# Performance work log

Hardware: AMD Instinct MI355X
Metric: run time of the kernel (lower is better)

## Reference

```python
import jax, jax.numpy as jnp
import numpy as np

N, E, D, D_NODE, D_EDGE, T, L = 100000, 640000, 128, 128, 32, 8, 3
EPS = 1e-5


def _layernorm(x, g, b):
    m = jnp.mean(x, -1, keepdims=True)
    v = jnp.mean((x - m) ** 2, -1, keepdims=True)
    return (x - m) * jax.lax.rsqrt(v + EPS) * g + b


def setup_inputs() -> dict:
    key = jax.random.key(0)
    ks = jax.random.split(key, 24)
    s = 0.02
    inp = {
        "x": jax.random.normal(ks[0], (N, D_NODE), jnp.float32),
        "edge_index": jax.random.randint(ks[1], (2, E), 0, N, jnp.int64),
        "edge_attr": jax.random.normal(ks[2], (E, D_EDGE), jnp.float32),
        "node_w": jax.random.normal(ks[3], (D_NODE, D), jnp.float32) * s,
        "node_b": jnp.zeros((D,), jnp.float32),
        "edge_w": jax.random.normal(ks[4], (D_EDGE, D), jnp.float32) * s,
        "edge_b": jnp.zeros((D,), jnp.float32),
        "msg_w1": jax.random.normal(ks[5], (L, D, D), jnp.float32) * s,
        "msg_b1": jnp.zeros((L, D), jnp.float32),
        "msg_w2": jax.random.normal(ks[6], (L, D, D), jnp.float32) * s,
        "msg_b2": jnp.zeros((L, D), jnp.float32),
        "upd_w1": jax.random.normal(ks[7], (L, D, 2 * D), jnp.float32) * s,
        "upd_b1": jnp.zeros((L, 2 * D), jnp.float32),
        "upd_w2": jax.random.normal(ks[8], (L, 2 * D, D), jnp.float32) * s,
        "upd_b2": jnp.zeros((L, D), jnp.float32),
        "ln_g": jnp.ones((L, D), jnp.float32),
        "ln_b": jnp.zeros((L, D), jnp.float32),
        "out_g": jnp.ones((D,), jnp.float32),
        "out_b": jnp.zeros((D,), jnp.float32),
    }
    return inp


def _pool_seg_ids():
    seg = T - 1
    cs = -(-N // seg)  # torch.chunk uses ceil chunk size
    sizes = []
    rem = N
    while rem > 0:
        sizes.append(min(cs, rem))
        rem -= cs
    return np.repeat(np.arange(len(sizes)), sizes), np.asarray(sizes, np.float32)


_SEG_IDS_NP, _SEG_SIZES_NP = _pool_seg_ids()


def reference(x, edge_index, edge_attr, node_w, node_b, edge_w, edge_b,
              msg_w1, msg_b1, msg_w2, msg_b2, upd_w1, upd_b1, upd_w2, upd_b2,
              ln_g, ln_b, out_g, out_b):
    node = x @ node_w + node_b                     # [N, D]
    edge_emb = edge_attr @ edge_w + edge_b         # [E, D]
    src, dst = edge_index[0], edge_index[1]
    deg = jax.ops.segment_sum(jnp.ones((E,), node.dtype), dst, num_segments=N)[:, None]
    deg = jnp.maximum(deg, 1.0)
    for i in range(L):
        h = jax.nn.gelu((node[src] + edge_emb) @ msg_w1[i] + msg_b1[i], approximate=False)
        msg = h @ msg_w2[i] + msg_b2[i]            # [E, D]
        agg = jax.ops.segment_sum(msg, dst, num_segments=N) / deg
        u = jax.nn.gelu(agg @ upd_w1[i] + upd_b1[i], approximate=False)
        u = u @ upd_w2[i] + upd_b2[i]
        node = _layernorm(node + u, ln_g[i], ln_b[i])
    # pooling: global mean token + (T-1) contiguous-segment means
    global_tok = node.mean(0, keepdims=True)       # [1, D]
    seg_ids = jnp.asarray(_SEG_IDS_NP)
    sums = jax.ops.segment_sum(node, seg_ids, num_segments=T - 1)
    seg_tok = sums / jnp.asarray(_SEG_SIZES_NP)[:, None]
    stacked = jnp.concatenate([global_tok, seg_tok], axis=0)  # [T, D]
    return _layernorm(stacked, out_g, out_b)
```

## Files before the change

### kernel.cpp

```cpp
#include <hip/hip_runtime.h>
#include <hip/hip_bf16.h>

#define N_NODES 100000
#define N_EDGES 640000
#define DD 128
#define DE 32
#define SCAN_B 256
#define SCAN_NB ((N_NODES + SCAN_B - 1) / SCAN_B)

typedef __attribute__((ext_vector_type(8))) short bf8v;
typedef __attribute__((ext_vector_type(4))) float f4v;

__device__ __forceinline__ float gelu_f(float x) {
    return 0.5f * x * (1.0f + erff(x * 0.70710678118654752f));
}
__device__ __forceinline__ float gelu_t(float x) {
    float x2 = x * x;
    float z = x * fmaf(0.1029437f, x2, 2.3022082f);
    float e = __builtin_amdgcn_exp2f(z);
    float r = __builtin_amdgcn_rcpf(e + 1.0f);
    return fmaf(-x, r, x);
}
__device__ __forceinline__ float bf2f(ushort u) {
    union { uint u; float f; } t; t.u = ((uint)u) << 16; return t.f;
}
__device__ __forceinline__ ushort f2bf(float f) {
    union { float f; uint u; } t; t.f = f;
    uint r = (t.u + 0x7fffu + ((t.u >> 16) & 1u)) >> 16;
    return (ushort)r;
}

template<int NW>
__device__ __forceinline__ void stage_w(ushort* lwgt, const ushort* __restrict__ src,
                                        int stride, int w, int lane) {
    constexpr int SEG = 32768 / NW;
#pragma unroll
    for (int k = 0; k < SEG / 1024; k++) {
        int o = w * SEG + k * 1024 + lane * 16;
        int row = o >> 8;
        int swz = o ^ ((row & 7) << 4);
        const ushort* g = src + (size_t)row * stride + ((swz & 255) >> 1);
        __builtin_amdgcn_global_load_lds(
            (const __attribute__((address_space(1))) void*)g,
            (__attribute__((address_space(3))) void*)(lwgt + (w * SEG + k * 1024) / 2),
            16, 0, 0);
    }
}

__device__ __forceinline__ void gemm_l(const bf8v* a, const ushort* lwgt,
                                       int cq, int quad, f4v* acc) {
    const char* lb = (const char*)lwgt;
    int sw = (cq & 7) << 4;
    __builtin_amdgcn_s_setprio(1);
#pragma unroll
    for (int ct = 0; ct < 8; ct++) {
#pragma unroll
        for (int kc = 0; kc < 4; kc++) {
            int addr = (((ct * 16 + cq) << 8) + (kc << 6) + (quad << 4)) ^ sw;
            acc[ct] = __builtin_amdgcn_mfma_f32_16x16x32_bf16(a[kc],
                *(const bf8v*)(lb + addr), acc[ct], 0, 0, 0);
        }
    }
    __builtin_amdgcn_s_setprio(0);
}

__global__ void k_count(const int* __restrict__ ei, int* __restrict__ cnt) {
    int e = blockIdx.x * blockDim.x + threadIdx.x;
    if (e < N_EDGES) atomicAdd(&cnt[ei[N_EDGES + e]], 1);
}

__global__ void k_scan1(const int* __restrict__ cnt, int* __restrict__ bsum) {
    __shared__ int s[SCAN_B];
    int i = blockIdx.x * SCAN_B + threadIdx.x;
    int v = (i < N_NODES) ? cnt[i] : 0;
    s[threadIdx.x] = v;
    __syncthreads();
    for (int off = SCAN_B / 2; off > 0; off >>= 1) {
        if (threadIdx.x < off) s[threadIdx.x] += s[threadIdx.x + off];
        __syncthreads();
    }
    if (threadIdx.x == 0) bsum[blockIdx.x] = s[0];
}

__global__ void k_scan2(int* __restrict__ bsum) {
    __shared__ int s[512];
    int t = threadIdx.x;
    int v = (t < SCAN_NB) ? bsum[t] : 0;
    s[t] = v;
    __syncthreads();
    for (int off = 1; off < 512; off <<= 1) {
        int u = (t >= off) ? s[t - off] : 0;
        __syncthreads();
        s[t] += u;
        __syncthreads();
    }
    if (t < SCAN_NB) bsum[t] = s[t] - v;
}

__global__ void k_scan3(const int* __restrict__ cnt, const int* __restrict__ bsum,
                        int* __restrict__ cursor, float* __restrict__ flag,
                        float* __restrict__ invdeg) {
    __shared__ int s[SCAN_B];
    int i = blockIdx.x * SCAN_B + threadIdx.x;
    int v = (i < N_NODES) ? cnt[i] : 0;
    s[threadIdx.x] = v;
    __syncthreads();
    for (int off = 1; off < SCAN_B; off <<= 1) {
        int u = (threadIdx.x >= off) ? s[threadIdx.x - off] : 0;
        __syncthreads();
        s[threadIdx.x] += u;
        __syncthreads();
    }
    if (i < N_NODES) {
        int excl = s[threadIdx.x] - v + bsum[blockIdx.x];
        cursor[i] = excl;
        flag[i] = (v > 0) ? 1.0f : 0.0f;
        invdeg[i] = (v > 0) ? 1.0f / (float)v : 0.0f;
    }
}

__global__ void k_scatter(const int* __restrict__ ei, int* __restrict__ cursor,
                          int* __restrict__ eord, int* __restrict__ esrc,
                          int* __restrict__ edst) {
    int e = blockIdx.x * blockDim.x + threadIdx.x;
    if (e < N_EDGES) {
        int d = ei[N_EDGES + e];
        int pos = atomicAdd(&cursor[d], 1);
        eord[pos] = e;
        esrc[pos] = ei[e];
        edst[pos] = d;
    }
}

__global__ void k_eperm(const int* __restrict__ eord, const float* __restrict__ ea,
                        ushort* __restrict__ eat) {
    int slot = blockIdx.x * 32 + (threadIdx.x >> 3);
    int l8 = threadIdx.x & 7;
    int e = eord[slot];
    const float* s = ea + (size_t)e * DE + l8 * 4;
    float4 v = *(const float4*)s;
    ushort4 o;
    o.x = f2bf(v.x); o.y = f2bf(v.y); o.z = f2bf(v.z); o.w = f2bf(v.w);
    *(ushort4*)(eat + (size_t)slot * DE + l8 * 4) = o;
}

__global__ void k_prep(const float* __restrict__ edge_w, const float* __restrict__ edge_b,
                       const float* __restrict__ msg_w1, const float* __restrict__ msg_b1,
                       ushort* __restrict__ WeT, float* __restrict__ bc) {
    int j = threadIdx.x;
    int c = blockIdx.x;
    int l = blockIdx.y;
    const float* w1 = msg_w1 + (size_t)l * DD * DD;
    if (c < DE) {
        float s = 0.0f;
        for (int k = 0; k < DD; k++) s += edge_w[c*DD + k] * w1[k*DD + j];
        WeT[((size_t)l*DD + j)*DE + c] = f2bf(s);
    } else {
        float s = msg_b1[l*DD + j];
        for (int k = 0; k < DD; k++) s += edge_b[k] * w1[k*DD + j];
        bc[l*DD + j] = s;
    }
}

struct TDesc { const float* src; ushort* dst; int R; int C; };
struct TPack { TDesc d[13]; };

__global__ void k_tball(TPack p) {
    TDesc t = p.d[blockIdx.y];
    int idx = blockIdx.x * 256 + threadIdx.x;
    if (idx < t.R * t.C) {
        int r = idx / t.C, c = idx % t.C;
        t.dst[(size_t)c * t.R + r] = f2bf(t.src[idx]);
    }
}

__global__ __launch_bounds__(256, 3) void k_embed(
    const float* __restrict__ x, const ushort* __restrict__ WT,
    const float* __restrict__ bias, const ushort* __restrict__ W1T,
    float* __restrict__ node, ushort* __restrict__ slotA, int M)
{
    __shared__ __align__(16) ushort lwgt[16384];
    __shared__ ushort tr[4][16 * 136];
    int tid = threadIdx.x, lane = tid & 63, w = tid >> 6;
    int base = (blockIdx.x * 4 + w) * 16;
    bool act = base < M;
    int cq = lane & 15, quad = lane >> 4;
    ushort* trw = tr[w];
    f4v acc[8];
    bf8v a[4];

    stage_w<4>(lwgt, WT, DD, w, lane);
    if (act) {
        const float* Af = x + (size_t)(base + cq) * DD;
#pragma unroll
        for (int kc = 0; kc < 4; kc++) {
            float4 v0 = *(const float4*)(Af + kc * 32 + quad * 8);
            float4 v1 = *(const float4*)(Af + kc * 32 + quad * 8 + 4);
            bf8v t;
            t[0]=(short)f2bf(v0.x); t[1]=(short)f2bf(v0.y); t[2]=(short)f2bf(v0.z); t[3]=(short)f2bf(v0.w);
            t[4]=(short)f2bf(v1.x); t[5]=(short)f2bf(v1.y); t[6]=(short)f2bf(v1.z); t[7]=(short)f2bf(v1.w);
            a[kc] = t;
        }
    }
    __syncthreads();
    int r0 = base + quad * 4;
    bf8v a2[4];
    if (act) {
#pragma unroll
        for (int ct = 0; ct < 8; ct++) acc[ct] = 0.0f;
        gemm_l(a, lwgt, cq, quad, acc);
#pragma unroll
        for (int ct = 0; ct < 8; ct++) {
            int col = ct * 16 + cq;
            float b_ = bias[col];
#pragma unroll
            for (int i = 0; i < 4; i++) {
                float v = acc[ct][i] + b_;
                node[(size_t)(r0 + i) * DD + col] = v;
                trw[(quad * 4 + i) * 136 + col] = f2bf(v);
            }
        }
#pragma unroll
        for (int kc = 0; kc < 4; kc++)
            a2[kc] = *(const bf8v*)(trw + cq * 136 + kc * 32 + quad * 8);
    }
    __syncthreads();
    stage_w<4>(lwgt, W1T, DD, w, lane);
    __syncthreads();
    if (act) {
#pragma unroll
        for (int ct = 0; ct < 8; ct++) acc[ct] = 0.0f;
        gemm_l(a2, lwgt, cq, quad, acc);
#pragma unroll
        for (int ct = 0; ct < 8; ct++) {
            int col = ct * 16 + cq;
#pragma unroll
            for (int i = 0; i < 4; i++)
                slotA[(size_t)(r0 + i) * DD + col] = f2bf(acc[ct][i]);
        }
    }
}

__global__ __launch_bounds__(256) void k_msg(
    const ushort* __restrict__ eat,
    const ushort* __restrict__ WeT, const float* __restrict__ bcv,
    const int* __restrict__ esrc, const int* __restrict__ edst,
    const ushort* __restrict__ slotA, float* __restrict__ aggf)
{
    __shared__ ushort tr[4][16 * 136];
    __shared__ int2 sd[4][16];
    int tid = threadIdx.x, lane = tid & 63, w = tid >> 6;
    int jt = (blockIdx.x * 4 + w) * 16;
    int cq = lane & 15, quad = lane >> 4;
    ushort* trw = tr[w];

    if (lane < 16) {
        int2 v; v.x = esrc[jt + lane]; v.y = edst[jt + lane];
        sd[w][lane] = v;
    }
    {
        bf8v a = *(const bf8v*)(eat + (size_t)(jt + cq) * DE + quad * 8);
        __builtin_amdgcn_s_setprio(1);
#pragma unroll
        for (int ct = 0; ct < 8; ct++) {
            bf8v b = *(const bf8v*)(WeT + (size_t)(ct * 16 + cq) * DE + quad * 8);
            f4v z; z = 0.0f;
            f4v r = __builtin_amdgcn_mfma_f32_16x16x32_bf16(a, b, z, 0, 0, 0);
            int col = ct * 16 + cq;
            float b_ = bcv[col];
#pragma unroll
            for (int i = 0; i < 4; i++)
                trw[(quad * 4 + i) * 136 + col] = f2bf(r[i] + b_);
        }
        __builtin_amdgcn_s_setprio(0);
    }
    float a0 = 0.0f, a1 = 0.0f;
    int rstart = 0;
#pragma unroll
    for (int r = 0; r < 16; r++) {
        int2 s = sd[w][r];
        uint em = *(const uint*)(trw + r * 136 + 2 * lane);
        uint nw = *(const uint*)(slotA + (size_t)s.x * DD + 2 * lane);
        a0 += gelu_t(bf2f((ushort)(em & 0xffffu)) + bf2f((ushort)(nw & 0xffffu)));
        a1 += gelu_t(bf2f((ushort)(em >> 16)) + bf2f((ushort)(nw >> 16)));
        bool flush = (r == 15) || (sd[w][r + 1].y != s.y);
        if (flush) {
            float* p = aggf + (size_t)s.y * DD + 2 * lane;
            if (rstart > 0 && r < 15) {
                float2 st; st.x = a0; st.y = a1;
                *(float2*)p = st;
            } else {
                atomicAdd(p, a0);
                atomicAdd(p + 1, a1);
            }
            a0 = 0.0f; a1 = 0.0f; rstart = r + 1;
        }
    }
}

template<int FUSE>
__global__ __launch_bounds__(256, 3) void k_mlp(
    float* __restrict__ aggf, const float* __restrict__ invdeg,
    const ushort* __restrict__ w2T, const float* __restrict__ b2,
    const float* __restrict__ flag,
    const ushort* __restrict__ u1T, const float* __restrict__ bu1,
    const ushort* __restrict__ u2T, const float* __restrict__ bu2,
    float* __restrict__ node,
    const float* __restrict__ lg, const float* __restrict__ lb,
    const ushort* __restrict__ w1nT, ushort* __restrict__ slotA, int M)
{
    __shared__ __align__(16) ushort lwgt[16384];
    __shared__ ushort tr[4][16 * 136];
    int tid = threadIdx.x, lane = tid & 63, w = tid >> 6;
    int base = (blockIdx.x * 4 + w) * 16;
    bool act = base < M;
    int cq = lane & 15, quad = lane >> 4;
    ushort* trw = tr[w];
    f4v acc[8];
    bf8v a[4], a2[4];

    stage_w<4>(lwgt, w2T, DD, w, lane);
    if (act) {
        float iv = invdeg[base + cq];
        float* Af = aggf + (size_t)(base + cq) * DD;
#pragma unroll
        for (int kc = 0; kc < 4; kc++) {
            float4 v0 = *(const float4*)(Af + kc * 32 + quad * 8);
            float4 v1 = *(const float4*)(Af + kc * 32 + quad * 8 + 4);
            bf8v t;
            t[0]=(short)f2bf(v0.x*iv); t[1]=(short)f2bf(v0.y*iv);
            t[2]=(short)f2bf(v0.z*iv); t[3]=(short)f2bf(v0.w*iv);
            t[4]=(short)f2bf(v1.x*iv); t[5]=(short)f2bf(v1.y*iv);
            t[6]=(short)f2bf(v1.z*iv); t[7]=(short)f2bf(v1.w*iv);
            a[kc] = t;
        }
        if (FUSE) {
            float4 z4; z4.x = 0.0f; z4.y = 0.0f; z4.z = 0.0f; z4.w = 0.0f;
#pragma unroll
            for (int kc = 0; kc < 4; kc++) {
                *(float4*)(Af + kc * 32 + quad * 8) = z4;
                *(float4*)(Af + kc * 32 + quad * 8 + 4) = z4;
            }
        }
    }
    __syncthreads();
    if (act) {
#pragma unroll
        for (int ct = 0; ct < 8; ct++) acc[ct] = 0.0f;
        gemm_l(a, lwgt, cq, quad, acc);
        float fl[4];
#pragma unroll
        for (int i = 0; i < 4; i++) fl[i] = flag[base + quad * 4 + i];
#pragma unroll
        for (int ct = 0; ct < 8; ct++) {
            int col = ct * 16 + cq;
            float b_ = b2[col];
#pragma unroll
            for (int i = 0; i < 4; i++)
                trw[(quad * 4 + i) * 136 + col] = f2bf(acc[ct][i] + fl[i] * b_);
        }
#pragma unroll
        for (int kc = 0; kc < 4; kc++)
            a2[kc] = *(const bf8v*)(trw + cq * 136 + kc * 32 + quad * 8);
    }

    f4v accU[8];
#pragma unroll
    for (int ct = 0; ct < 8; ct++) accU[ct] = 0.0f;
#pragma unroll
    for (int h = 0; h < 2; h++) {
        __syncthreads();
        stage_w<4>(lwgt, u1T + (size_t)h * 128 * DD, DD, w, lane);
        __syncthreads();
        bf8v tf[4];
        if (act) {
#pragma unroll
            for (int ct = 0; ct < 8; ct++) acc[ct] = 0.0f;
            gemm_l(a2, lwgt, cq, quad, acc);
#pragma unroll
            for (int ct = 0; ct < 8; ct++) {
                int col = ct * 16 + cq;
                float b_ = bu1[h * 128 + col];
#pragma unroll
                for (int i = 0; i < 4; i++)
                    trw[(quad * 4 + i) * 136 + col] = f2bf(gelu_f(acc[ct][i] + b_));
            }
#pragma unroll
            for (int kc = 0; kc < 4; kc++)
                tf[kc] = *(const bf8v*)(trw + cq * 136 + kc * 32 + quad * 8);
        }
        __syncthreads();
        stage_w<4>(lwgt, u2T + (size_t)h * 128, 256, w, lane);
        __syncthreads();
        if (act) gemm_l(tf, lwgt, cq, quad, accU);
    }

    int r0 = base + quad * 4;
    if (act) {
        float xv[8][4], lgc[8], lbc[8];
#pragma unroll
        for (int ct = 0; ct < 8; ct++) {
            int col = ct * 16 + cq;
            float b_ = bu2[col];
            lgc[ct] = lg[col]; lbc[ct] = lb[col];
#pragma unroll
            for (int i = 0; i < 4; i++)
                xv[ct][i] = accU[ct][i] + b_ + node[(size_t)(r0 + i) * DD + col];
        }
#pragma unroll
        for (int i = 0; i < 4; i++) {
            float s = 0.0f;
#pragma unroll
            for (int ct = 0; ct < 8; ct++) s += xv[ct][i];
            s += __shfl_xor(s, 1); s += __shfl_xor(s, 2);
            s += __shfl_xor(s, 4); s += __shfl_xor(s, 8);
            float m = s * (1.0f / 128.0f);
            float vv = 0.0f;
#pragma unroll
            for (int ct = 0; ct < 8; ct++) { float d = xv[ct][i] - m; vv += d * d; }
            vv += __shfl_xor(vv, 1); vv += __shfl_xor(vv, 2);
            vv += __shfl_xor(vv, 4); vv += __shfl_xor(vv, 8);
            float inv = rsqrtf(vv * (1.0f / 128.0f) + 1e-5f);
#pragma unroll
            for (int ct = 0; ct < 8; ct++) {
                int col = ct * 16 + cq;
                float y = (xv[ct][i] - m) * inv * lgc[ct] + lbc[ct];
                node[(size_t)(r0 + i) * DD + col] = y;
                if (FUSE) trw[(quad * 4 + i) * 136 + col] = f2bf(y);
            }
        }
    }

    if (FUSE) {
        __syncthreads();
        stage_w<4>(lwgt, w1nT, DD, w, lane);
        __syncthreads();
        if (act) {
            bf8v nf[4];
#pragma unroll
            for (int kc = 0; kc < 4; kc++)
                nf[kc] = *(const bf8v*)(trw + cq * 136 + kc * 32 + quad * 8);
#pragma unroll
            for (int ct = 0; ct < 8; ct++) acc[ct] = 0.0f;
            gemm_l(nf, lwgt, cq, quad, acc);
#pragma unroll
            for (int ct = 0; ct < 8; ct++) {
                int col = ct * 16 + cq;
#pragma unroll
                for (int i = 0; i < 4; i++)
                    slotA[(size_t)(r0 + i) * DD + col] = f2bf(acc[ct][i]);
            }
        }
    }
}

__global__ void k_pool_partial(const float* __restrict__ node, float* __restrict__ partial) {
    int seg = blockIdx.x, chunk = blockIdx.y, j = threadIdx.x;
    int segbase = seg * 14286;
    int segcnt = (seg == 6) ? 14284 : 14286;
    const int per = 112;
    int lo = chunk * per, hi = min(lo + per, segcnt);
    float s = 0.0f;
    for (int r = lo; r < hi; r++) s += node[(size_t)(segbase + r) * DD + j];
    partial[(size_t)(seg * 128 + chunk) * DD + j] = s;
}

__global__ void k_pool_final(const float* __restrict__ partial, const float* __restrict__ g,
                             const float* __restrict__ b, float* __restrict__ out) {
    __shared__ float red[128];
    int j = threadIdx.x;
    float tok[8];
    float tot = 0.0f;
#pragma unroll
    for (int s = 0; s < 7; s++) {
        float v = 0.0f;
        for (int c = 0; c < 128; c++) v += partial[(size_t)(s * 128 + c) * DD + j];
        tok[1 + s] = v / ((s == 6) ? 14284.0f : 14286.0f);
        tot += v;
    }
    tok[0] = tot / 100000.0f;
    for (int t = 0; t < 8; t++) {
        float x = tok[t];
        red[j] = x; __syncthreads();
        for (int off = 64; off > 0; off >>= 1) {
            if (j < off) red[j] += red[j + off];
            __syncthreads();
        }
        float m = red[0] / 128.0f;
        __syncthreads();
        float d = x - m;
        red[j] = d * d; __syncthreads();
        for (int off = 64; off > 0; off >>= 1) {
            if (j < off) red[j] += red[j + off];
            __syncthreads();
        }
        float var = red[0] / 128.0f;
        __syncthreads();
        out[t * DD + j] = d * rsqrtf(var + 1e-5f) * g[j] + b[j];
    }
}

extern "C" void kernel_launch(void* const* d_in, const int* in_sizes, int n_in,
                              void* d_out, int out_size, void* d_ws, size_t ws_size,
                              hipStream_t stream) {
    const float* x         = (const float*)d_in[0];
    const int*   ei        = (const int*)d_in[1];
    const float* edge_attr = (const float*)d_in[2];
    const float* node_w    = (const float*)d_in[3];
    const float* node_b    = (const float*)d_in[4];
    const float* edge_w    = (const float*)d_in[5];
    const float* edge_b    = (const float*)d_in[6];
    const float* msg_w1    = (const float*)d_in[7];
    const float* msg_b1    = (const float*)d_in[8];
    const float* msg_w2    = (const float*)d_in[9];
    const float* msg_b2    = (const float*)d_in[10];
    const float* upd_w1    = (const float*)d_in[11];
    const float* upd_b1    = (const float*)d_in[12];
    const float* upd_w2    = (const float*)d_in[13];
    const float* upd_b2    = (const float*)d_in[14];
    const float* ln_g      = (const float*)d_in[15];
    const float* ln_b      = (const float*)d_in[16];
    const float* out_g     = (const float*)d_in[17];
    const float* out_b     = (const float*)d_in[18];
    float* out = (float*)d_out;

    char* pw = (char*)d_ws;
    auto alloc = [&](size_t bytes) -> void* {
        void* r = (void*)pw;
        pw += (bytes + 255) & ~(size_t)255;
        return r;
    };
    float*  node_f  = (float*) alloc((size_t)N_NODES * DD * 4);
    ushort* slotA   = (ushort*)alloc((size_t)N_NODES * DD * 2);
    float*  aggf    = (float*) alloc((size_t)N_NODES * DD * 4);
    ushort* eat     = (ushort*)alloc((size_t)N_EDGES * DE * 2);
    float*  bc      = (float*) alloc((size_t)3 * DD * 4);
    ushort* WeT     = (ushort*)alloc((size_t)3 * DD * DE * 2);
    float*  partial = (float*) alloc((size_t)7 * 128 * DD * 4);
    float*  degflag = (float*) alloc((size_t)N_NODES * 4);
    float*  invdeg  = (float*) alloc((size_t)N_NODES * 4);
    ushort* node_wT = (ushort*)alloc((size_t)DD * DD * 2);
    ushort* msg_w1T = (ushort*)alloc((size_t)3 * DD * DD * 2);
    ushort* msg_w2T = (ushort*)alloc((size_t)3 * DD * DD * 2);
    ushort* upd_w1T = (ushort*)alloc((size_t)3 * 256 * DD * 2);
    ushort* upd_w2T = (ushort*)alloc((size_t)3 * DD * 256 * 2);
    int* cnt        = (int*)   alloc((size_t)N_NODES * 4);
    int* cursor     = (int*)   alloc((size_t)N_NODES * 4);
    int* bsum       = (int*)   alloc((size_t)512 * 4);
    int* eord       = (int*)   alloc((size_t)N_EDGES * 4);
    int* esrc       = (int*)   alloc((size_t)N_EDGES * 4);
    int* edst       = (int*)   alloc((size_t)N_EDGES * 4);

    hipMemsetAsync(cnt, 0, N_NODES * sizeof(int), stream);
    hipMemsetAsync(aggf, 0, (size_t)N_NODES * DD * 4, stream);
    k_count  <<<(N_EDGES + 255) / 256, 256, 0, stream>>>(ei, cnt);
    k_scan1  <<<SCAN_NB, SCAN_B, 0, stream>>>(cnt, bsum);
    k_scan2  <<<1, 512, 0, stream>>>(bsum);
    k_scan3  <<<SCAN_NB, SCAN_B, 0, stream>>>(cnt, bsum, cursor, degflag, invdeg);
    k_scatter<<<(N_EDGES + 255) / 256, 256, 0, stream>>>(ei, cursor, eord, esrc, edst);
    k_eperm  <<<N_EDGES / 32, 256, 0, stream>>>(eord, edge_attr, eat);
    k_prep   <<<dim3(DE + 1, 3), DD, 0, stream>>>(edge_w, edge_b, msg_w1, msg_b1, WeT, bc);

    TPack tp;
    tp.d[0] = { node_w, node_wT, DD, DD };
    for (int l = 0; l < 3; l++) {
        tp.d[1 + l*4 + 0] = { msg_w1 + (size_t)l*DD*DD,  msg_w1T + (size_t)l*DD*DD,  DD, DD };
        tp.d[1 + l*4 + 1] = { msg_w2 + (size_t)l*DD*DD,  msg_w2T + (size_t)l*DD*DD,  DD, DD };
        tp.d[1 + l*4 + 2] = { upd_w1 + (size_t)l*DD*256, upd_w1T + (size_t)l*256*DD, DD, 256 };
        tp.d[1 + l*4 + 3] = { upd_w2 + (size_t)l*256*DD, upd_w2T + (size_t)l*DD*256, 256, DD };
    }
    k_tball<<<dim3(128, 13), 256, 0, stream>>>(tp);

    const int GB = (N_NODES / 16 + 3) / 4;
    const int MSG_GB = N_EDGES / 64;
    k_embed<<<GB, 256, 0, stream>>>(x, node_wT, node_b, msg_w1T, node_f, slotA, N_NODES);

    for (int l = 0; l < 3; l++) {
        k_msg<<<MSG_GB, 256, 0, stream>>>(eat, WeT + (size_t)l*DD*DE,
            bc + (size_t)l*DD, esrc, edst, slotA, aggf);
        if (l < 2) {
            k_mlp<1><<<GB, 256, 0, stream>>>(aggf, invdeg,
                msg_w2T + (size_t)l*DD*DD, msg_b2 + (size_t)l*DD, degflag,
                upd_w1T + (size_t)l*256*DD, upd_b1 + (size_t)l*256,
                upd_w2T + (size_t)l*DD*256, upd_b2 + (size_t)l*DD,
                node_f, ln_g + (size_t)l*DD, ln_b + (size_t)l*DD,
                msg_w1T + (size_t)(l+1)*DD*DD, slotA, N_NODES);
        } else {
            k_mlp<0><<<GB, 256, 0, stream>>>(aggf, invdeg,
                msg_w2T + (size_t)l*DD*DD, msg_b2 + (size_t)l*DD, degflag,
                upd_w1T + (size_t)l*256*DD, upd_b1 + (size_t)l*256,
                upd_w2T + (size_t)l*DD*256, upd_b2 + (size_t)l*DD,
                node_f, ln_g + (size_t)l*DD, ln_b + (size_t)l*DD,
                msg_w1T, slotA, N_NODES);
        }
    }

    k_pool_partial<<<dim3(7, 128), DD, 0, stream>>>(node_f, partial);
    k_pool_final  <<<1, DD, 0, stream>>>(partial, out_g, out_b, out);
}
```

Measured before the change: 849.8 us.

## Process 32 rows per wave in node MLP, fuse edge permute into scatter

The node MLP kernel now handles two 16-row tiles per wave, so each weight tile staged in LDS is reused for twice as many rows, halving weight staging and barriers per row. Occupancy drops to 2 blocks per CU and register pressure rises. The edge-attribute permute/convert is folded into the scatter kernel, removing the eord buffer and one launch, but each thread now reads a full 128-byte row. The message kernel prefetches all 16 source-node gathers into registers before the GELU/accumulate loop to overlap memory latency.

Result: slower. 871.5 us (+2.6%).

```diff
diff --git a/kernel.cpp b/kernel.cpp
--- a/kernel.cpp
+++ b/kernel.cpp
@@ -119,29 +119,25 @@
     }
 }
 
-__global__ void k_scatter(const int* __restrict__ ei, int* __restrict__ cursor,
-                          int* __restrict__ eord, int* __restrict__ esrc,
-                          int* __restrict__ edst) {
+__global__ void k_scatter(const int* __restrict__ ei, const float* __restrict__ ea,
+                          int* __restrict__ cursor, int* __restrict__ esrc,
+                          int* __restrict__ edst, ushort* __restrict__ eat) {
     int e = blockIdx.x * blockDim.x + threadIdx.x;
     if (e < N_EDGES) {
         int d = ei[N_EDGES + e];
         int pos = atomicAdd(&cursor[d], 1);
-        eord[pos] = e;
         esrc[pos] = ei[e];
         edst[pos] = d;
-    }
-}
-
-__global__ void k_eperm(const int* __restrict__ eord, const float* __restrict__ ea,
-                        ushort* __restrict__ eat) {
-    int slot = blockIdx.x * 32 + (threadIdx.x >> 3);
-    int l8 = threadIdx.x & 7;
-    int e = eord[slot];
-    const float* s = ea + (size_t)e * DE + l8 * 4;
-    float4 v = *(const float4*)s;
-    ushort4 o;
-    o.x = f2bf(v.x); o.y = f2bf(v.y); o.z = f2bf(v.z); o.w = f2bf(v.w);
-    *(ushort4*)(eat + (size_t)slot * DE + l8 * 4) = o;
+        const float* s = ea + (size_t)e * DE;
+        ushort* o = eat + (size_t)pos * DE;
+#pragma unroll
+        for (int k = 0; k < 8; k++) {
+            float4 v = *(const float4*)(s + k * 4);
+            ushort4 u;
+            u.x = f2bf(v.x); u.y = f2bf(v.y); u.z = f2bf(v.z); u.w = f2bf(v.w);
+            *(ushort4*)(o + k * 4) = u;
+        }
+    }
 }
 
 __global__ void k_prep(const float* __restrict__ edge_w, const float* __restrict__ edge_b,
@@ -274,18 +270,22 @@
         }
         __builtin_amdgcn_s_setprio(0);
     }
+    uint nwv[16];
+#pragma unroll
+    for (int r = 0; r < 16; r++)
+        nwv[r] = *(const uint*)(slotA + (size_t)sd[w][r].x * DD + 2 * lane);
     float a0 = 0.0f, a1 = 0.0f;
     int rstart = 0;
 #pragma unroll
     for (int r = 0; r < 16; r++) {
-        int2 s = sd[w][r];
+        int dcur = sd[w][r].y;
         uint em = *(const uint*)(trw + r * 136 + 2 * lane);
-        uint nw = *(const uint*)(slotA + (size_t)s.x * DD + 2 * lane);
+        uint nw = nwv[r];
         a0 += gelu_t(bf2f((ushort)(em & 0xffffu)) + bf2f((ushort)(nw & 0xffffu)));
         a1 += gelu_t(bf2f((ushort)(em >> 16)) + bf2f((ushort)(nw >> 16)));
-        bool flush = (r == 15) || (sd[w][r + 1].y != s.y);
+        bool flush = (r == 15) || (sd[w][r + 1].y != dcur);
         if (flush) {
-            float* p = aggf + (size_t)s.y * DD + 2 * lane;
+            float* p = aggf + (size_t)dcur * DD + 2 * lane;
             if (rstart > 0 && r < 15) {
                 float2 st; st.x = a0; st.y = a1;
                 *(float2*)p = st;
@@ -299,7 +299,7 @@
 }
 
 template<int FUSE>
-__global__ __launch_bounds__(256, 3) void k_mlp(
+__global__ __launch_bounds__(256, 2) void k_mlp(
     float* __restrict__ aggf, const float* __restrict__ invdeg,
     const ushort* __restrict__ w2T, const float* __restrict__ b2,
     const float* __restrict__ flag,
@@ -310,45 +310,59 @@
     const ushort* __restrict__ w1nT, ushort* __restrict__ slotA, int M)
 {
     __shared__ __align__(16) ushort lwgt[16384];
-    __shared__ ushort tr[4][16 * 136];
+    __shared__ ushort tr[4][2][16 * 136];
     int tid = threadIdx.x, lane = tid & 63, w = tid >> 6;
-    int base = (blockIdx.x * 4 + w) * 16;
+    int base = (blockIdx.x * 4 + w) * 32;
     bool act = base < M;
     int cq = lane & 15, quad = lane >> 4;
-    ushort* trw = tr[w];
-    f4v acc[8];
-    bf8v a[4], a2[4];
+    ushort* trw0 = tr[w][0];
+    ushort* trw1 = tr[w][1];
+    f4v acc[8], accU0[8], accU1[8];
+    bf8v a2_0[4], a2_1[4];
 
     stage_w<4>(lwgt, w2T, DD, w, lane);
+    bf8v a0[4], a1[4];
     if (act) {
-        float iv = invdeg[base + cq];
-        float* Af = aggf + (size_t)(base + cq) * DD;
+        float iv0 = invdeg[base + cq];
+        float iv1 = invdeg[base + 16 + cq];
+        float* Af0 = aggf + (size_t)(base + cq) * DD;
+        float* Af1 = aggf + (size_t)(base + 16 + cq) * DD;
 #pragma unroll
         for (int kc = 0; kc < 4; kc++) {
-            float4 v0 = *(const float4*)(Af + kc * 32 + quad * 8);
-            float4 v1 = *(const float4*)(Af + kc * 32 + quad * 8 + 4);
+            float4 v0 = *(const float4*)(Af0 + kc * 32 + quad * 8);
+            float4 v1 = *(const float4*)(Af0 + kc * 32 + quad * 8 + 4);
             bf8v t;
-            t[0]=(short)f2bf(v0.x*iv); t[1]=(short)f2bf(v0.y*iv);
-            t[2]=(short)f2bf(v0.z*iv); t[3]=(short)f2bf(v0.w*iv);
-            t[4]=(short)f2bf(v1.x*iv); t[5]=(short)f2bf(v1.y*iv);
-            t[6]=(short)f2bf(v1.z*iv); t[7]=(short)f2bf(v1.w*iv);
-            a[kc] = t;
+            t[0]=(short)f2bf(v0.x*iv0); t[1]=(short)f2bf(v0.y*iv0);
+            t[2]=(short)f2bf(v0.z*iv0); t[3]=(short)f2bf(v0.w*iv0);
+            t[4]=(short)f2bf(v1.x*iv0); t[5]=(short)f2bf(v1.y*iv0);
+            t[6]=(short)f2bf(v1.z*iv0); t[7]=(short)f2bf(v1.w*iv0);
+            a0[kc] = t;
+            float4 w0 = *(const float4*)(Af1 + kc * 32 + quad * 8);
+            float4 w1 = *(const float4*)(Af1 + kc * 32 + quad * 8 + 4);
+            bf8v s;
+            s[0]=(short)f2bf(w0.x*iv1); s[1]=(short)f2bf(w0.y*iv1);
+            s[2]=(short)f2bf(w0.z*iv1); s[3]=(short)f2bf(w0.w*iv1);
+            s[4]=(short)f2bf(w1.x*iv1); s[5]=(short)f2bf(w1.y*iv1);
+            s[6]=(short)f2bf(w1.z*iv1); s[7]=(short)f2bf(w1.w*iv1);
+            a1[kc] = s;
         }
         if (FUSE) {
             float4 z4; z4.x = 0.0f; z4.y = 0.0f; z4.z = 0.0f; z4.w = 0.0f;
 #pragma unroll
             for (int kc = 0; kc < 4; kc++) {
-                *(float4*)(Af + kc * 32 + quad * 8) = z4;
-                *(float4*)(Af + kc * 32 + quad * 8 + 4) = z4;
+                *(float4*)(Af0 + kc * 32 + quad * 8) = z4;
+                *(float4*)(Af0 + kc * 32 + quad * 8 + 4) = z4;
+                *(float4*)(Af1 + kc * 32 + quad * 8) = z4;
+                *(float4*)(Af1 + kc * 32 + quad * 8 + 4) = z4;
             }
         }
     }
     __syncthreads();
     if (act) {
+        float fl[4];
 #pragma unroll
         for (int ct = 0; ct < 8; ct++) acc[ct] = 0.0f;
-        gemm_l(a, lwgt, cq, quad, acc);
-        float fl[4];
+        gemm_l(a0, lwgt, cq, quad, acc);
 #pragma unroll
         for (int i = 0; i < 4; i++) fl[i] = flag[base + quad * 4 + i];
 #pragma unroll
@@ -357,76 +371,145 @@
             float b_ = b2[col];
 #pragma unroll
             for (int i = 0; i < 4; i++)
-                trw[(quad * 4 + i) * 136 + col] = f2bf(acc[ct][i] + fl[i] * b_);
+                trw0[(quad * 4 + i) * 136 + col] = f2bf(acc[ct][i] + fl[i] * b_);
         }
 #pragma unroll
         for (int kc = 0; kc < 4; kc++)
-            a2[kc] = *(const bf8v*)(trw + cq * 136 + kc * 32 + quad * 8);
-    }
-
-    f4v accU[8];
-#pragma unroll
-    for (int ct = 0; ct < 8; ct++) accU[ct] = 0.0f;
+            a2_0[kc] = *(const bf8v*)(trw0 + cq * 136 + kc * 32 + quad * 8);
+#pragma unroll
+        for (int ct = 0; ct < 8; ct++) acc[ct] = 0.0f;
+        gemm_l(a1, lwgt, cq, quad, acc);
+#pragma unroll
+        for (int i = 0; i < 4; i++) fl[i] = flag[base + 16 + quad * 4 + i];
+#pragma unroll
+        for (int ct = 0; ct < 8; ct++) {
+            int col = ct * 16 + cq;
+            float b_ = b2[col];
+#pragma unroll
+            for (int i = 0; i < 4; i++)
+                trw1[(quad * 4 + i) * 136 + col] = f2bf(acc[ct][i] + fl[i] * b_);
+        }
+#pragma unroll
+        for (int kc = 0; kc < 4; kc++)
+            a2_1[kc] = *(const bf8v*)(trw1 + cq * 136 + kc * 32 + quad * 8);
+    }
+
+#pragma unroll
+    for (int ct = 0; ct < 8; ct++) { accU0[ct] = 0.0f; accU1[ct] = 0.0f; }
 #pragma unroll
     for (int h = 0; h < 2; h++) {
         __syncthreads();
         stage_w<4>(lwgt, u1T + (size_t)h * 128 * DD, DD, w, lane);
         __syncthreads();
-        bf8v tf[4];
         if (act) {
 #pragma unroll
             for (int ct = 0; ct < 8; ct++) acc[ct] = 0.0f;
-            gemm_l(a2, lwgt, cq, quad, acc);
+            gemm_l(a2_0, lwgt, cq, quad, acc);
 #pragma unroll
             for (int ct = 0; ct < 8; ct++) {
                 int col = ct * 16 + cq;
                 float b_ = bu1[h * 128 + col];
 #pragma unroll
                 for (int i = 0; i < 4; i++)
-                    trw[(quad * 4 + i) * 136 + col] = f2bf(gelu_f(acc[ct][i] + b_));
-            }
-#pragma unroll
-            for (int kc = 0; kc < 4; kc++)
-                tf[kc] = *(const bf8v*)(trw + cq * 136 + kc * 32 + quad * 8);
-        }
-        __syncthreads();
-        stage_w<4>(lwgt, u2T + (size_t)h * 128, 256, w, lane);
-        __syncthreads();
-        if (act) gemm_l(tf, lwgt, cq, quad, accU);
-    }
-
-    int r0 = base + quad * 4;
-    if (act) {
-        float xv[8][4], lgc[8], lbc[8];
-#pragma unroll
-        for (int ct = 0; ct < 8; ct++) {
-            int col = ct * 16 + cq;
-            float b_ = bu2[col];
-            lgc[ct] = lg[col]; lbc[ct] = lb[col];
-#pragma unroll
-            for (int i = 0; i < 4; i++)
-                xv[ct][i] = accU[ct][i] + b_ + node[(size_t)(r0 + i) * DD + col];
-        }
-#pragma unroll
-        for (int i = 0; i < 4; i++) {
-            float s = 0.0f;
-#pragma unroll
-            for (int ct = 0; ct < 8; ct++) s += xv[ct][i];
-            s += __shfl_xor(s, 1); s += __shfl_xor(s, 2);
-            s += __shfl_xor(s, 4); s += __shfl_xor(s, 8);
-            float m = s * (1.0f / 128.0f);
-            float vv = 0.0f;
-#pragma unroll
-            for (int ct = 0; ct < 8; ct++) { float d = xv[ct][i] - m; vv += d * d; }
-            vv += __shfl_xor(vv, 1); vv += __shfl_xor(vv, 2);
-            vv += __shfl_xor(vv, 4); vv += __shfl_xor(vv, 8);
-            float inv = rsqrtf(vv * (1.0f / 128.0f) + 1e-5f);
+                    trw0[(quad * 4 + i) * 136 + col] = f2bf(gelu_f(acc[ct][i] + b_));
+            }
+#pragma unroll
+            for (int ct = 0; ct < 8; ct++) acc[ct] = 0.0f;
+            gemm_l(a2_1, lwgt, cq, quad, acc);
 #pragma unroll
             for (int ct = 0; ct < 8; ct++) {
                 int col = ct * 16 + cq;
-                float y = (xv[ct][i] - m) * inv * lgc[ct] + lbc[ct];
-                node[(size_t)(r0 + i) * DD + col] = y;
-                if (FUSE) trw[(quad * 4 + i) * 136 + col] = f2bf(y);
+                float b_ = bu1[h * 128 + col];
+#pragma unroll
+                for (int i = 0; i < 4; i++)
+                    trw1[(quad * 4 + i) * 136 + col] = f2bf(gelu_f(acc[ct][i] + b_));
+            }
+        }
+        __syncthreads();
+        stage_w<4>(lwgt, u2T + (size_t)h * 128, 256, w, lane);
+        __syncthreads();
+        if (act) {
+            bf8v tf[4];
+#pragma unroll
+            for (int kc = 0; kc < 4; kc++)
+                tf[kc] = *(const bf8v*)(trw0 + cq * 136 + kc * 32 + quad * 8);
+            gemm_l(tf, lwgt, cq, quad, accU0);
+#pragma unroll
+            for (int kc = 0; kc < 4; kc++)
+                tf[kc] = *(const bf8v*)(trw1 + cq * 136 + kc * 32 + quad * 8);
+            gemm_l(tf, lwgt, cq, quad, accU1);
+        }
+    }
+
+    if (act) {
+        {
+            int r0 = base + quad * 4;
+            float xv[8][4], lgc[8], lbc[8];
+#pragma unroll
+            for (int ct = 0; ct < 8; ct++) {
+                int col = ct * 16 + cq;
+                float b_ = bu2[col];
+                lgc[ct] = lg[col]; lbc[ct] = lb[col];
+#pragma unroll
+                for (int i = 0; i < 4; i++)
+                    xv[ct][i] = accU0[ct][i] + b_ + node[(size_t)(r0 + i) * DD + col];
+            }
+#pragma unroll
+            for (int i = 0; i < 4; i++) {
+                float s = 0.0f;
+#pragma unroll
+                for (int ct = 0; ct < 8; ct++) s += xv[ct][i];
+                s += __shfl_xor(s, 1); s += __shfl_xor(s, 2);
+                s += __shfl_xor(s, 4); s += __shfl_xor(s, 8);
+                float m = s * (1.0f / 128.0f);
+                float vv = 0.0f;
+#pragma unroll
+                for (int ct = 0; ct < 8; ct++) { float d = xv[ct][i] - m; vv += d * d; }
+                vv += __shfl_xor(vv, 1); vv += __shfl_xor(vv, 2);
+                vv += __shfl_xor(vv, 4); vv += __shfl_xor(vv, 8);
+                float inv = rsqrtf(vv * (1.0f / 128.0f) + 1e-5f);
+#pragma unroll
+                for (int ct = 0; ct < 8; ct++) {
+                    int col = ct * 16 + cq;
+                    float y = (xv[ct][i] - m) * inv * lgc[ct] + lbc[ct];
+                    node[(size_t)(r0 + i) * DD + col] = y;
+                    if (FUSE) trw0[(quad * 4 + i) * 136 + col] = f2bf(y);
+                }
+            }
+        }
+        {
+            int r0 = base + 16 + quad * 4;
+            float xv[8][4], lgc[8], lbc[8];
+#pragma unroll
+            for (int ct = 0; ct < 8; ct++) {
+                int col = ct * 16 + cq;
+                float b_ = bu2[col];
+                lgc[ct] = lg[col]; lbc[ct] = lb[col];
+#pragma unroll
+                for (int i = 0; i < 4; i++)
+                    xv[ct][i] = accU1[ct][i] + b_ + node[(size_t)(r0 + i) * DD + col];
+            }
+#pragma unroll
+            for (int i = 0; i < 4; i++) {
+                float s = 0.0f;
+#pragma unroll
+                for (int ct = 0; ct < 8; ct++) s += xv[ct][i];
+                s += __shfl_xor(s, 1); s += __shfl_xor(s, 2);
+                s += __shfl_xor(s, 4); s += __shfl_xor(s, 8);
+                float m = s * (1.0f / 128.0f);
+                float vv = 0.0f;
+#pragma unroll
+                for (int ct = 0; ct < 8; ct++) { float d = xv[ct][i] - m; vv += d * d; }
+                vv += __shfl_xor(vv, 1); vv += __shfl_xor(vv, 2);
+                vv += __shfl_xor(vv, 4); vv += __shfl_xor(vv, 8);
+                float inv = rsqrtf(vv * (1.0f / 128.0f) + 1e-5f);
+#pragma unroll
+                for (int ct = 0; ct < 8; ct++) {
+                    int col = ct * 16 + cq;
+                    float y = (xv[ct][i] - m) * inv * lgc[ct] + lbc[ct];
+                    node[(size_t)(r0 + i) * DD + col] = y;
+                    if (FUSE) trw1[(quad * 4 + i) * 136 + col] = f2bf(y);
+                }
             }
         }
     }
@@ -439,16 +522,31 @@
             bf8v nf[4];
 #pragma unroll
             for (int kc = 0; kc < 4; kc++)
-                nf[kc] = *(const bf8v*)(trw + cq * 136 + kc * 32 + quad * 8);
+                nf[kc] = *(const bf8v*)(trw0 + cq * 136 + kc * 32 + quad * 8);
 #pragma unroll
             for (int ct = 0; ct < 8; ct++) acc[ct] = 0.0f;
             gemm_l(nf, lwgt, cq, quad, acc);
+            int r0 = base + quad * 4;
 #pragma unroll
             for (int ct = 0; ct < 8; ct++) {
                 int col = ct * 16 + cq;
 #pragma unroll
                 for (int i = 0; i < 4; i++)
                     slotA[(size_t)(r0 + i) * DD + col] = f2bf(acc[ct][i]);
+            }
+#pragma unroll
+            for (int kc = 0; kc < 4; kc++)
+                nf[kc] = *(const bf8v*)(trw1 + cq * 136 + kc * 32 + quad * 8);
+#pragma unroll
+            for (int ct = 0; ct < 8; ct++) acc[ct] = 0.0f;
+            gemm_l(nf, lwgt, cq, quad, acc);
+            int r1 = base + 16 + quad * 4;
+#pragma unroll
+            for (int ct = 0; ct < 8; ct++) {
+                int col = ct * 16 + cq;
+#pragma unroll
+                for (int i = 0; i < 4; i++)
+                    slotA[(size_t)(r1 + i) * DD + col] = f2bf(acc[ct][i]);
             }
         }
     }
@@ -547,7 +645,6 @@
     int* cnt        = (int*)   alloc((size_t)N_NODES * 4);
     int* cursor     = (int*)   alloc((size_t)N_NODES * 4);
     int* bsum       = (int*)   alloc((size_t)512 * 4);
-    int* eord       = (int*)   alloc((size_t)N_EDGES * 4);
     int* esrc       = (int*)   alloc((size_t)N_EDGES * 4);
     int* edst       = (int*)   alloc((size_t)N_EDGES * 4);
 
@@ -557,8 +654,7 @@
     k_scan1  <<<SCAN_NB, SCAN_B, 0, stream>>>(cnt, bsum);
     k_scan2  <<<1, 512, 0, stream>>>(bsum);
     k_scan3  <<<SCAN_NB, SCAN_B, 0, stream>>>(cnt, bsum, cursor, degflag, invdeg);
-    k_scatter<<<(N_EDGES + 255) / 256, 256, 0, stream>>>(ei, cursor, eord, esrc, edst);
-    k_eperm  <<<N_EDGES / 32, 256, 0, stream>>>(eord, edge_attr, eat);
+    k_scatter<<<(N_EDGES + 255) / 256, 256, 0, stream>>>(ei, edge_attr, cursor, esrc, edst, eat);
     k_prep   <<<dim3(DE + 1, 3), DD, 0, stream>>>(edge_w, edge_b, msg_w1, msg_b1, WeT, bc);
 
     TPack tp;
@@ -572,6 +668,7 @@
     k_tball<<<dim3(128, 13), 256, 0, stream>>>(tp);
 
     const int GB = (N_NODES / 16 + 3) / 4;
+    const int GB32 = (N_NODES / 32 + 3) / 4;
     const int MSG_GB = N_EDGES / 64;
     k_embed<<<GB, 256, 0, stream>>>(x, node_wT, node_b, msg_w1T, node_f, slotA, N_NODES);
 
@@ -579,14 +676,14 @@
         k_msg<<<MSG_GB, 256, 0, stream>>>(eat, WeT + (size_t)l*DD*DE,
             bc + (size_t)l*DD, esrc, edst, slotA, aggf);
         if (l < 2) {
-            k_mlp<1><<<GB, 256, 0, stream>>>(aggf, invdeg,
+            k_mlp<1><<<GB32, 256, 0, stream>>>(aggf, invdeg,
                 msg_w2T + (size_t)l*DD*DD, msg_b2 + (size_t)l*DD, degflag,
                 upd_w1T + (size_t)l*256*DD, upd_b1 + (size_t)l*256,
                 upd_w2T + (size_t)l*DD*256, upd_b2 + (size_t)l*DD,
                 node_f, ln_g + (size_t)l*DD, ln_b + (size_t)l*DD,
                 msg_w1T + (size_t)(l+1)*DD*DD, slotA, N_NODES);
         } else {
-            k_mlp<0><<<GB, 256, 0, stream>>>(aggf, invdeg,
+            k_mlp<0><<<GB32, 256, 0, stream>>>(aggf, invdeg,
                 msg_w2T + (size_t)l*DD*DD, msg_b2 + (size_t)l*DD, degflag,
                 upd_w1T + (size_t)l*256*DD, upd_b1 + (size_t)l*256,
                 upd_w2T + (size_t)l*DD*256, upd_b2 + (size_t)l*DD,
```
